# Optimization experiments

Hardware: AMD Instinct MI355X
Metric: run time of the kernel (lower is better)

Reference implementation:

```python
import jax, jax.numpy as jnp
import numpy as np

B, T, F, H = 256, 512, 64, 128


def _uniform(key, shape, stdv):
    return jax.random.uniform(key, shape, jnp.float32, -stdv, stdv)


def setup_inputs() -> dict:
    key = jax.random.key(0)
    ks = jax.random.split(key, 24)
    values = jax.random.normal(ks[0], (B, T, F), jnp.float32)
    masks = (jax.random.uniform(ks[1], (B, T, F)) < 0.8).astype(jnp.float32)
    deltas = jax.random.uniform(ks[2], (B, T, F), jnp.float32)
    labels = (jax.random.uniform(ks[3], (B, 1)) < 0.5).astype(jnp.float32)
    is_train = (jax.random.uniform(ks[4], (B, 1)) < 0.8).astype(jnp.float32)
    sH = 1.0 / np.sqrt(H)
    sF = 1.0 / np.sqrt(F)
    # temp_decay_h: Linear F -> H (stdv = 1/sqrt(out) per reset_parameters)
    W_dh = _uniform(ks[5], (H, F), sH); b_dh = _uniform(ks[6], (H,), sH)
    # temp_decay_x: diag F -> F
    W_dx = _uniform(ks[7], (F, F), sF); b_dx = _uniform(ks[8], (F,), sF)
    # hist_reg: Linear H -> F (torch Linear stdv = 1/sqrt(in))
    W_hr = _uniform(ks[9], (F, H), sH); b_hr = _uniform(ks[10], (F,), sH)
    # feat_reg: F -> F with zeroed diagonal mask
    W_fr = _uniform(ks[11], (F, F), sF); b_fr = _uniform(ks[12], (F,), sF)
    # weight_combine: Linear 2F -> F
    s2F = 1.0 / np.sqrt(2 * F)
    W_wc = _uniform(ks[13], (F, 2 * F), s2F); b_wc = _uniform(ks[14], (F,), s2F)
    # LSTMCell(2F, H): torch init uniform(-1/sqrt(H), 1/sqrt(H)), gate order i,f,g,o
    W_ih = _uniform(ks[15], (4 * H, 2 * F), sH); b_ih = _uniform(ks[16], (4 * H,), sH)
    W_hh = _uniform(ks[17], (4 * H, H), sH); b_hh = _uniform(ks[18], (4 * H,), sH)
    # out: Linear H -> 1
    W_out = _uniform(ks[19], (1, H), sH); b_out = _uniform(ks[20], (1,), sH)
    return dict(values=values, masks=masks, deltas=deltas, labels=labels, is_train=is_train,
                W_dh=W_dh, b_dh=b_dh, W_dx=W_dx, b_dx=b_dx, W_hr=W_hr, b_hr=b_hr,
                W_fr=W_fr, b_fr=b_fr, W_wc=W_wc, b_wc=b_wc,
                W_ih=W_ih, b_ih=b_ih, W_hh=W_hh, b_hh=b_hh, W_out=W_out, b_out=b_out)


def _forward(values, masks, deltas, labels, is_train,
             W_dh, b_dh, W_dx, b_dx, W_hr, b_hr, W_fr, b_fr, W_wc, b_wc,
             W_ih, b_ih, W_hh, b_hh, W_out, b_out):
    eps = 1e-5
    w_dx_diag = jnp.diagonal(W_dx)            # diag mask: W * I
    W_fr_m = W_fr * (1.0 - jnp.eye(F, dtype=W_fr.dtype))  # zero diagonal

    def step(carry, xs):
        h, c, x_loss = carry
        x, m, d = xs                           # each [B, F]
        gamma_h = jnp.exp(-jax.nn.relu(d @ W_dh.T + b_dh))   # [B, H]
        gamma_x = jnp.exp(-jax.nn.relu(d * w_dx_diag + b_dx))  # [B, F]
        h = h * gamma_h
        x_h = h @ W_hr.T + b_hr                # [B, F]
        msum = jnp.sum(m) + eps
        x_loss = x_loss + jnp.sum(jnp.abs(x - x_h) * m) / msum
        x_c = m * x + (1.0 - m) * x_h
        z_h = x_c @ W_fr_m.T + b_fr
        x_loss = x_loss + jnp.sum(jnp.abs(x - z_h) * m) / msum
        alpha = jnp.concatenate([gamma_x, m], axis=1) @ W_wc.T + b_wc
        c_h = alpha * z_h + (1.0 - alpha) * x_h
        x_loss = x_loss + jnp.sum(jnp.abs(x - c_h) * m) / msum
        c_c = m * x + (1.0 - m) * c_h
        inp = jnp.concatenate([c_c, m], axis=1)   # [B, 2F]
        gates = inp @ W_ih.T + b_ih + h @ W_hh.T + b_hh  # [B, 4H]
        i, f, g, o = jnp.split(gates, 4, axis=1)
        c = jax.nn.sigmoid(f) * c + jax.nn.sigmoid(i) * jnp.tanh(g)
        h = jax.nn.sigmoid(o) * jnp.tanh(c)
        return (h, c, x_loss), c_c

    h0 = jnp.zeros((values.shape[0], H), values.dtype)
    c0 = jnp.zeros((values.shape[0], H), values.dtype)
    xs = (jnp.swapaxes(values, 0, 1), jnp.swapaxes(masks, 0, 1), jnp.swapaxes(deltas, 0, 1))
    (h, c, x_loss), imps = jax.lax.scan(step, (h0, c0, jnp.float32(0.0)), xs)
    imputations = jnp.swapaxes(imps, 0, 1)     # [B, T, F]
    y_h = h @ W_out.T + b_out                  # [B, 1] logits
    # stable BCE with logits (matches torch reference formula)
    max_val = jnp.maximum(-y_h, 0.0)
    y_l = y_h - y_h * labels + max_val + jnp.log(jnp.exp(-max_val) + jnp.exp(-y_h - max_val))
    y_loss = jnp.sum(y_l * is_train) / (jnp.sum(is_train) + eps)
    loss = x_loss / T + y_loss * 0.3
    predictions = jax.nn.sigmoid(y_h)
    return loss, predictions, imputations


def reference(values, masks, deltas, labels, is_train,
              W_dh, b_dh, W_dx, b_dx, W_hr, b_hr, W_fr, b_fr, W_wc, b_wc,
              W_ih, b_ih, W_hh, b_hh, W_out, b_out):
    return _forward(values, masks, deltas, labels, is_train,
                    W_dh, b_dh, W_dx, b_dx, W_hr, b_hr, W_fr, b_fr, W_wc, b_wc,
                    W_ih, b_ih, W_hh, b_hh, W_out, b_out)
```

## Files before the change

### kernel.cpp

```cpp
#include <hip/hip_runtime.h>
#include <hip/hip_fp16.h>


#define NBATCH 256
#define NT 512
#define NF 64
#define NH 128

#define WHH_OFF   0u
#define WIH_OFF   131072u
#define WHR_OFF   262144u
#define WFR_OFF   278528u
#define INVMS_OFF 286720u
#define ISTR_OFF  288768u
#define GH_OFF    294912u
#define AL_OFF    33849344u

typedef _Float16 half2_t __attribute__((ext_vector_type(2)));

__device__ __forceinline__ unsigned pack2(float a, float b) {
    __half2 h = __floats2half2_rn(a, b);
    return __builtin_bit_cast(unsigned, h);
}

__device__ __forceinline__ float dot2f(unsigned w, unsigned a, float acc) {
#if __has_builtin(__builtin_amdgcn_fdot2)
    return __builtin_amdgcn_fdot2(__builtin_bit_cast(half2_t, w),
                                  __builtin_bit_cast(half2_t, a), acc, false);
#else
    float2 wf = __half22float2(__builtin_bit_cast(__half2, w));
    float2 af = __half22float2(__builtin_bit_cast(__half2, a));
    return acc + wf.x * af.x + wf.y * af.y;
#endif
}

__device__ __forceinline__ float sigm(float x) { return 1.f / (1.f + __expf(-x)); }
__device__ __forceinline__ float tanh_fast(float x) { return 1.f - 2.f / (__expf(2.f * x) + 1.f); }

__global__ __launch_bounds__(256) void prep_w(const float* __restrict__ Whh,
                                              const float* __restrict__ Wih,
                                              const float* __restrict__ Whr,
                                              const float* __restrict__ Wfr,
                                              unsigned* __restrict__ wsu) {
    int o = blockIdx.x * 256 + threadIdx.x;
    float v0, v1;
    if (o < 32768) {
        int c = o & 3, r = (o >> 2) & 511, cb = o >> 11;
        int col = 8 * cb + 2 * c;
        v0 = Whh[r * 128 + col]; v1 = Whh[r * 128 + col + 1];
    } else if (o < 65536) {
        int o2 = o - 32768;
        int c = o2 & 3, r = (o2 >> 2) & 511, cb = o2 >> 11;
        int col = 8 * cb + 2 * c;
        v0 = Wih[r * 128 + col]; v1 = Wih[r * 128 + col + 1];
    } else if (o < 69632) {
        int o3 = o - 65536;
        int c = o3 & 3, f = (o3 >> 2) & 63, cb = o3 >> 8;
        int col = 8 * cb + 2 * c;
        v0 = Whr[f * 128 + col]; v1 = Whr[f * 128 + col + 1];
    } else if (o < 71680) {
        int o4 = o - 69632;
        int c = o4 & 3, f = (o4 >> 2) & 63, cb = o4 >> 8;
        int col = 8 * cb + 2 * c;
        v0 = (col == f) ? 0.f : Wfr[f * 64 + col];
        v1 = (col + 1 == f) ? 0.f : Wfr[f * 64 + col + 1];
    } else {
        return;
    }
    wsu[o] = pack2(v0, v1);
}

__global__ __launch_bounds__(256) void prep_msum(const float* __restrict__ masks,
                                                 const float* __restrict__ is_train,
                                                 float* __restrict__ invms,
                                                 float* __restrict__ inv_istr,
                                                 float* __restrict__ d_out0) {
    __shared__ float red[256];
    int tid = threadIdx.x;
    int t = blockIdx.x;
    if (t < NT) {
        int f = tid & 63, br = tid >> 6;
        float s = 0.f;
        for (int i = 0; i < 64; i++) {
            int b = br + i * 4;
            s += masks[((size_t)b * NT + t) * NF + f];
        }
        red[tid] = s;
        __syncthreads();
        for (int off = 128; off > 0; off >>= 1) {
            if (tid < off) red[tid] += red[tid + off];
            __syncthreads();
        }
        if (tid == 0) invms[t] = 1.f / (red[0] + 1e-5f);
    } else {
        red[tid] = is_train[tid];
        __syncthreads();
        for (int off = 128; off > 0; off >>= 1) {
            if (tid < off) red[tid] += red[tid + off];
            __syncthreads();
        }
        if (tid == 0) {
            *inv_istr = 1.f / (red[0] + 1e-5f);
            *d_out0 = 0.f;
        }
    }
}

__global__ __launch_bounds__(256) void ga_kernel(const float* __restrict__ deltas,
                                                 const float* __restrict__ masks,
                                                 const float* __restrict__ Wdh,
                                                 const float* __restrict__ bdh,
                                                 const float* __restrict__ Wdx,
                                                 const float* __restrict__ bdx,
                                                 const float* __restrict__ Wwc,
                                                 const float* __restrict__ bwc,
                                                 __half* __restrict__ gh_all,
                                                 __half* __restrict__ al_all) {
    __shared__ unsigned wdhpk[32 * 128];
    __shared__ unsigned wwcpk[64 * 64];
    __shared__ float sbdh[128], sbdx[64], swdx[64], sbwc[64];
    __shared__ float dbuf[64];
    __shared__ __align__(16) unsigned dpk[32], gxpk[32], mpk2[32];
    int tid = threadIdx.x;

    for (int o = tid; o < 4096; o += 256) {
        int j = o & 127, k2 = o >> 7;
        wdhpk[o] = pack2(Wdh[j * 64 + 2 * k2], Wdh[j * 64 + 2 * k2 + 1]);
    }
    for (int o = tid; o < 4096; o += 256) {
        int f = o & 63, k2 = o >> 6;
        wwcpk[o] = pack2(Wwc[f * 128 + 2 * k2], Wwc[f * 128 + 2 * k2 + 1]);
    }
    if (tid < 128) sbdh[tid] = bdh[tid];
    if (tid < 64) {
        sbdx[tid] = bdx[tid];
        swdx[tid] = Wdx[tid * 65];
        sbwc[tid] = bwc[tid];
    }
    __syncthreads();

    for (int i = 0; i < 32; i++) {
        int p = blockIdx.x * 32 + i;
        if (tid < 32) {
            float2 dv = ((const float2*)(deltas + (size_t)p * NF))[tid];
            dbuf[2 * tid] = dv.x; dbuf[2 * tid + 1] = dv.y;
            dpk[tid] = pack2(dv.x, dv.y);
        } else if (tid < 64) {
            int q = tid - 32;
            float2 mv = ((const float2*)(masks + (size_t)p * NF))[q];
            mpk2[q] = pack2(mv.x, mv.y);
        }
        __syncthreads();
        if (tid < 64) {
            float gx = __expf(-fmaxf(dbuf[tid] * swdx[tid] + sbdx[tid], 0.f));
            float oth = __shfl_xor(gx, 1);
            if (!(tid & 1)) gxpk[tid >> 1] = pack2(gx, oth);
        }
        __syncthreads();
        if (tid < 128) {
            float a0 = sbdh[tid], a1 = 0.f;
            #pragma unroll
            for (int k8 = 0; k8 < 8; k8++) {
                uint4 dp = *(const uint4*)&dpk[4 * k8];
                a0 = dot2f(wdhpk[(4 * k8 + 0) * 128 + tid], dp.x, a0);
                a1 = dot2f(wdhpk[(4 * k8 + 1) * 128 + tid], dp.y, a1);
                a0 = dot2f(wdhpk[(4 * k8 + 2) * 128 + tid], dp.z, a0);
                a1 = dot2f(wdhpk[(4 * k8 + 3) * 128 + tid], dp.w, a1);
            }
            gh_all[(size_t)p * NH + tid] = __float2half(__expf(-fmaxf(a0 + a1, 0.f)));
        } else if (tid < 192) {
            int f = tid - 128;
            float a0 = sbwc[f], a1 = 0.f;
            #pragma unroll
            for (int k8 = 0; k8 < 8; k8++) {
                uint4 gp = *(const uint4*)&gxpk[4 * k8];
                a0 = dot2f(wwcpk[(4 * k8 + 0) * 64 + f], gp.x, a0);
                a1 = dot2f(wwcpk[(4 * k8 + 1) * 64 + f], gp.y, a1);
                a0 = dot2f(wwcpk[(4 * k8 + 2) * 64 + f], gp.z, a0);
                a1 = dot2f(wwcpk[(4 * k8 + 3) * 64 + f], gp.w, a1);
            }
            #pragma unroll
            for (int k8 = 0; k8 < 8; k8++) {
                uint4 mp = *(const uint4*)&mpk2[4 * k8];
                a0 = dot2f(wwcpk[(32 + 4 * k8 + 0) * 64 + f], mp.x, a0);
                a1 = dot2f(wwcpk[(32 + 4 * k8 + 1) * 64 + f], mp.y, a1);
                a0 = dot2f(wwcpk[(32 + 4 * k8 + 2) * 64 + f], mp.z, a0);
                a1 = dot2f(wwcpk[(32 + 4 * k8 + 3) * 64 + f], mp.w, a1);
            }
            al_all[(size_t)p * NF + f] = __float2half(a0 + a1);
        }
        __syncthreads();
    }
}

__global__ __launch_bounds__(512, 2) void main_kernel(
    const float* __restrict__ values, const float* __restrict__ masks,
    const float* __restrict__ labels, const float* __restrict__ is_train,
    const float* __restrict__ b_hr, const float* __restrict__ b_fr,
    const float* __restrict__ b_ih, const float* __restrict__ b_hh,
    const float* __restrict__ W_out, const float* __restrict__ b_out,
    const uint4* __restrict__ whh_ws, const uint4* __restrict__ wih_ws,
    const uint4* __restrict__ whr_ws, const uint4* __restrict__ wfr_ws,
    const float* __restrict__ invms, const float* __restrict__ inv_istr,
    const __half* __restrict__ gh_all, const __half* __restrict__ al_all,
    float* __restrict__ d_out) {
    __shared__ uint4 wfr4[8 * 64];
    __shared__ float sbhr[64], sbfr[64];
    __shared__ __align__(16) unsigned hpk[64];
    __shared__ float xp[512];
    __shared__ float mbuf[64], xbuf[64], albuf[64];
    __shared__ __align__(16) unsigned mpk[32], xcpk[32], ccpk[32];
    __shared__ __align__(16) unsigned ghpk[64];
    __shared__ float hfin[128];
    __shared__ float sinvt;

    const int tid = threadIdx.x;
    const int b = blockIdx.x;
    const int s = tid & 3;
    const int cq = tid >> 2;
    const int kg = tid >> 6;
    const int fl = tid & 63;

    uint4 whh_q[16];
    uint4 wihc_q[8];
    uint4 wihm_q[8];
    float bg4[4];
    #pragma unroll
    for (int g = 0; g < 4; g++) {
        int r = g * 128 + cq;
        #pragma unroll
        for (int j = 0; j < 4; j++) whh_q[g * 4 + j] = whh_ws[(4 * s + j) * 512 + r];
        #pragma unroll
        for (int j = 0; j < 2; j++) {
            wihc_q[g * 2 + j] = wih_ws[(2 * s + j) * 512 + r];
            wihm_q[g * 2 + j] = wih_ws[(8 + 2 * s + j) * 512 + r];
        }
        bg4[g] = b_ih[r] + b_hh[r];
    }
    uint4 whr_pa = whr_ws[(2 * kg) * 64 + fl];
    uint4 whr_pb = whr_ws[(2 * kg + 1) * 64 + fl];
    wfr4[tid] = wfr_ws[tid];
    if (tid < 64) { sbhr[tid] = b_hr[tid]; sbfr[tid] = b_fr[tid]; hpk[tid] = 0u; }

    const float* vp = values + (size_t)b * NT * NF;
    const float* mp = masks + (size_t)b * NT * NF;
    const __half* alp = al_all + (size_t)b * NT * NF;
    const unsigned* ghu = (const unsigned*)(gh_all + (size_t)b * NT * NH);
    float* imp = d_out + 257 + (size_t)b * NT * NF;

    float creg = 0.f;
    float lloss = 0.f;
    float hacc4[4] = {0.f, 0.f, 0.f, 0.f};
    float macc4[4] = {0.f, 0.f, 0.f, 0.f};

    float xn = 0.f, aln = 0.f, invtn = 0.f;
    float2 mn = make_float2(0.f, 0.f);
    unsigned ghA = 0u, ghB = 0u;
    if (tid >= 256 && tid < 320) {
        int q = tid - 256;
        xn = vp[q];
        aln = __half2float(alp[q]);
        if (q == 0) invtn = invms[0];
    } else if (tid >= 320 && tid < 352) {
        mn = ((const float2*)mp)[tid - 320];
    } else if (tid >= 352 && tid < 416) {
        int q = tid - 352;
        ghA = ghu[64 + q];
        ghB = ghu[128 + q];
    }
    __syncthreads();

    for (int t = 0; t < NT; t++) {
        if (tid >= 256 && tid < 320) {
            int q = tid - 256;
            xbuf[q] = xn; albuf[q] = aln;
            if (q == 0) sinvt = invtn;
        } else if (tid >= 320 && tid < 352) {
            int q = tid - 320;
            mbuf[2 * q] = mn.x; mbuf[2 * q + 1] = mn.y;
            mpk[q] = pack2(mn.x, mn.y);
        }
        {
            int tn = (t + 1 < NT) ? (t + 1) : (NT - 1);
            if (tid >= 256 && tid < 320) {
                int q = tid - 256;
                xn = vp[tn * NF + q];
                aln = __half2float(alp[tn * NF + q]);
                if (q == 0) invtn = invms[tn];
            } else if (tid >= 320 && tid < 352) {
                mn = ((const float2*)(mp + tn * NF))[tid - 320];
            }
        }
        #pragma unroll
        for (int g = 0; g < 4; g++) {
            float u0 = 0.f, u1 = 0.f;
            #pragma unroll
            for (int j = 0; j < 4; j++) {
                uint4 hq = *(const uint4*)&hpk[16 * s + 4 * j];
                uint4 w = whh_q[g * 4 + j];
                u0 = dot2f(w.x, hq.x, u0); u1 = dot2f(w.y, hq.y, u1);
                u0 = dot2f(w.z, hq.z, u0); u1 = dot2f(w.w, hq.w, u1);
            }
            hacc4[g] = u0 + u1;
        }
        {
            uint4 hpa = *(const uint4*)&hpk[8 * kg];
            uint4 hpb = *(const uint4*)&hpk[8 * kg + 4];
            float p0, p1;
            p0 = dot2f(whr_pa.x, hpa.x, 0.f); p1 = dot2f(whr_pa.y, hpa.y, 0.f);
            p0 = dot2f(whr_pa.z, hpa.z, p0);  p1 = dot2f(whr_pa.w, hpa.w, p1);
            p0 = dot2f(whr_pb.x, hpb.x, p0);  p1 = dot2f(whr_pb.y, hpb.y, p1);
            p0 = dot2f(whr_pb.z, hpb.z, p0);  p1 = dot2f(whr_pb.w, hpb.w, p1);
            xp[tid] = p0 + p1;
        }
        __syncthreads();

        if (tid < 64) {
            __builtin_amdgcn_s_setprio(1);
            float xh = sbhr[fl];
            #pragma unroll
            for (int g8 = 0; g8 < 8; g8++) xh += xp[g8 * 64 + fl];
            float xv = xbuf[fl], mv = mbuf[fl], av = albuf[fl], it = sinvt;
            float xc = mv * xv + (1.f - mv) * xh;
            float oth = __shfl_xor(xc, 1);
            if (!(fl & 1)) xcpk[fl >> 1] = pack2(xc, oth);
            float b0 = sbfr[fl], b1 = 0.f;
            #pragma unroll
            for (int k4 = 0; k4 < 8; k4++) {
                uint4 w = wfr4[k4 * 64 + fl];
                uint4 xq = *(const uint4*)&xcpk[4 * k4];
                b0 = dot2f(w.x, xq.x, b0); b1 = dot2f(w.y, xq.y, b1);
                b0 = dot2f(w.z, xq.z, b0); b1 = dot2f(w.w, xq.w, b1);
            }
            float zh = b0 + b1;
            float ch = av * zh + (1.f - av) * xh;
            float cc = mv * xv + (1.f - mv) * ch;
            imp[t * NF + fl] = cc;
            lloss += (fabsf(xv - xh) + fabsf(xv - zh) + fabsf(xv - ch)) * mv * it;
            oth = __shfl_xor(cc, 1);
            if (!(fl & 1)) ccpk[fl >> 1] = pack2(cc, oth);
            __builtin_amdgcn_s_setprio(0);
        } else {
            if (tid >= 352 && tid < 416) {
                int q = tid - 352;
                ghpk[q] = ghA;
                ghA = ghB;
                int tg = (t + 3 < NT) ? (t + 3) : (NT - 1);
                ghB = ghu[(size_t)tg * 64 + q];
            }
            uint4 mq0 = *(const uint4*)&mpk[8 * s];
            uint4 mq1 = *(const uint4*)&mpk[8 * s + 4];
            #pragma unroll
            for (int g = 0; g < 4; g++) {
                uint4 wa = wihm_q[g * 2], wb = wihm_q[g * 2 + 1];
                float u0 = dot2f(wa.x, mq0.x, 0.f), u1 = dot2f(wa.y, mq0.y, 0.f);
                u0 = dot2f(wa.z, mq0.z, u0); u1 = dot2f(wa.w, mq0.w, u1);
                u0 = dot2f(wb.x, mq1.x, u0); u1 = dot2f(wb.y, mq1.y, u1);
                u0 = dot2f(wb.z, mq1.z, u0); u1 = dot2f(wb.w, mq1.w, u1);
                macc4[g] = u0 + u1;
            }
        }
        __syncthreads();

        {
            if (tid < 64) {
                uint4 mq0 = *(const uint4*)&mpk[8 * s];
                uint4 mq1 = *(const uint4*)&mpk[8 * s + 4];
                #pragma unroll
                for (int g = 0; g < 4; g++) {
                    uint4 wa = wihm_q[g * 2], wb = wihm_q[g * 2 + 1];
                    float u0 = dot2f(wa.x, mq0.x, 0.f), u1 = dot2f(wa.y, mq0.y, 0.f);
                    u0 = dot2f(wa.z, mq0.z, u0); u1 = dot2f(wa.w, mq0.w, u1);
                    u0 = dot2f(wb.x, mq1.x, u0); u1 = dot2f(wb.y, mq1.y, u1);
                    u0 = dot2f(wb.z, mq1.z, u0); u1 = dot2f(wb.w, mq1.w, u1);
                    macc4[g] = u0 + u1;
                }
            }
            uint4 cq0 = *(const uint4*)&ccpk[8 * s];
            uint4 cq1 = *(const uint4*)&ccpk[8 * s + 4];
            float gate[4];
            #pragma unroll
            for (int g = 0; g < 4; g++) {
                uint4 wa = wihc_q[g * 2], wb = wihc_q[g * 2 + 1];
                float u0 = dot2f(wa.x, cq0.x, 0.f), u1 = dot2f(wa.y, cq0.y, 0.f);
                u0 = dot2f(wa.z, cq0.z, u0); u1 = dot2f(wa.w, cq0.w, u1);
                u0 = dot2f(wb.x, cq1.x, u0); u1 = dot2f(wb.y, cq1.y, u1);
                u0 = dot2f(wb.z, cq1.z, u0); u1 = dot2f(wb.w, cq1.w, u1);
                float v = hacc4[g] + macc4[g] + (u0 + u1);
                v += __shfl_xor(v, 1);
                v += __shfl_xor(v, 2);
                gate[g] = v + bg4[g];
            }
            float cn = sigm(gate[1]) * creg + sigm(gate[0]) * tanh_fast(gate[2]);
            creg = cn;
            float hn = sigm(gate[3]) * tanh_fast(cn);
            float gm = __half2float(((const __half*)ghpk)[cq]);
            float hd = hn * gm;
            float oth = __shfl_xor(hd, 4);
            if (!(tid & 7)) hpk[tid >> 3] = pack2(hd, oth);
            if (t == NT - 1 && !(tid & 3)) hfin[cq] = hn;
        }
        __syncthreads();
    }

    if (tid < 64) {
        float ll = lloss;
        float yp = hfin[tid] * W_out[tid] + hfin[64 + tid] * W_out[64 + tid];
        #pragma unroll
        for (int off = 32; off > 0; off >>= 1) {
            ll += __shfl_down(ll, off);
            yp += __shfl_down(yp, off);
        }
        if (tid == 0) {
            float yh = yp + b_out[0];
            d_out[1 + b] = 1.f / (1.f + expf(-yh));
            float lab = labels[b], istr = is_train[b];
            float maxv = fmaxf(-yh, 0.f);
            float yl = yh - yh * lab + maxv + logf(expf(-maxv) + expf(-yh - maxv));
            atomicAdd(d_out, ll * (1.f / (float)NT) + 0.3f * yl * istr * (*inv_istr));
        }
    }
}

extern "C" void kernel_launch(void* const* d_in, const int* in_sizes, int n_in,
                              void* d_out, int out_size, void* d_ws, size_t ws_size,
                              hipStream_t stream) {
    const float* values = (const float*)d_in[0];
    const float* masks = (const float*)d_in[1];
    const float* deltas = (const float*)d_in[2];
    const float* labels = (const float*)d_in[3];
    const float* is_train = (const float*)d_in[4];
    const float* W_dh = (const float*)d_in[5];
    const float* b_dh = (const float*)d_in[6];
    const float* W_dx = (const float*)d_in[7];
    const float* b_dx = (const float*)d_in[8];
    const float* W_hr = (const float*)d_in[9];
    const float* b_hr = (const float*)d_in[10];
    const float* W_fr = (const float*)d_in[11];
    const float* b_fr = (const float*)d_in[12];
    const float* W_wc = (const float*)d_in[13];
    const float* b_wc = (const float*)d_in[14];
    const float* W_ih = (const float*)d_in[15];
    const float* b_ih = (const float*)d_in[16];
    const float* W_hh = (const float*)d_in[17];
    const float* b_hh = (const float*)d_in[18];
    const float* W_out = (const float*)d_in[19];
    const float* b_out = (const float*)d_in[20];

    char* ws = (char*)d_ws;
    unsigned* wsu = (unsigned*)d_ws;
    const uint4* whh_ws = (const uint4*)(ws + WHH_OFF);
    const uint4* wih_ws = (const uint4*)(ws + WIH_OFF);
    const uint4* whr_ws = (const uint4*)(ws + WHR_OFF);
    const uint4* wfr_ws = (const uint4*)(ws + WFR_OFF);
    float* invms = (float*)(ws + INVMS_OFF);
    float* inv_istr = (float*)(ws + ISTR_OFF);
    __half* gh_all = (__half*)(ws + GH_OFF);
    __half* al_all = (__half*)(ws + AL_OFF);
    float* out_f = (float*)d_out;

    prep_w<<<280, 256, 0, stream>>>(W_hh, W_ih, W_hr, W_fr, wsu);
    prep_msum<<<513, 256, 0, stream>>>(masks, is_train, invms, inv_istr, out_f);
    ga_kernel<<<4096, 256, 0, stream>>>(deltas, masks, W_dh, b_dh, W_dx, b_dx,
                                        W_wc, b_wc, gh_all, al_all);
    main_kernel<<<NBATCH, 512, 0, stream>>>(values, masks, labels, is_train,
                                            b_hr, b_fr, b_ih, b_hh, W_out, b_out,
                                            whh_ws, wih_ws, whr_ws, wfr_ws,
                                            invms, inv_istr, gh_all, al_all, out_f);
}
```

Measured before the change: 1.372 ms.

## Unroll timestep loop by four with batched input staging and DPP reductions

After: 1.289 ms. 1.06x faster.

```diff
diff --git a/kernel.cpp b/kernel.cpp
--- a/kernel.cpp
+++ b/kernel.cpp
@@ -36,6 +36,19 @@
 
 __device__ __forceinline__ float sigm(float x) { return 1.f / (1.f + __expf(-x)); }
 __device__ __forceinline__ float tanh_fast(float x) { return 1.f - 2.f / (__expf(2.f * x) + 1.f); }
+
+__device__ __forceinline__ float quad_add_x1(float v) {
+    int r = __builtin_amdgcn_update_dpp(0, __builtin_bit_cast(int, v),
+                                        0xB1 , 0xF, 0xF, true);
+    return v + __builtin_bit_cast(float, r);
+}
+__device__ __forceinline__ float quad_add_x2(float v) {
+    int r = __builtin_amdgcn_update_dpp(0, __builtin_bit_cast(int, v),
+                                        0x4E , 0xF, 0xF, true);
+    return v + __builtin_bit_cast(float, r);
+}
+
+#define KEEP4(u) asm volatile("" : "+v"(u.x), "+v"(u.y), "+v"(u.z), "+v"(u.w))
 
 __global__ __launch_bounds__(256) void prep_w(const float* __restrict__ Whh,
                                               const float* __restrict__ Wih,
@@ -206,13 +219,14 @@
     float* __restrict__ d_out) {
     __shared__ uint4 wfr4[8 * 64];
     __shared__ float sbhr[64], sbfr[64];
-    __shared__ __align__(16) unsigned hpk[64];
+    __shared__ __align__(16) __half hph[128];
     __shared__ float xp[512];
-    __shared__ float mbuf[64], xbuf[64], albuf[64];
-    __shared__ __align__(16) unsigned mpk[32], xcpk[32], ccpk[32];
-    __shared__ __align__(16) unsigned ghpk[64];
+    __shared__ float xbuf4[4][64], albuf4[4][64], mbuf4[4][64];
+    __shared__ __align__(16) unsigned mpk4[4][32];
+    __shared__ __align__(16) __half xcph[64], ccph[64];
+    __shared__ __align__(16) unsigned ghpk4[4][64];
+    __shared__ float invt4[4];
     __shared__ float hfin[128];
-    __shared__ float sinvt;
 
     const int tid = threadIdx.x;
     const int b = blockIdx.x;
@@ -240,7 +254,8 @@
     uint4 whr_pa = whr_ws[(2 * kg) * 64 + fl];
     uint4 whr_pb = whr_ws[(2 * kg + 1) * 64 + fl];
     wfr4[tid] = wfr_ws[tid];
-    if (tid < 64) { sbhr[tid] = b_hr[tid]; sbfr[tid] = b_fr[tid]; hpk[tid] = 0u; }
+    if (tid < 64) { sbhr[tid] = b_hr[tid]; sbfr[tid] = b_fr[tid]; }
+    if (tid < 128) hph[tid] = __float2half(0.f);
 
     const float* vp = values + (size_t)b * NT * NF;
     const float* mp = masks + (size_t)b * NT * NF;
@@ -252,120 +267,152 @@
     float lloss = 0.f;
     float hacc4[4] = {0.f, 0.f, 0.f, 0.f};
     float macc4[4] = {0.f, 0.f, 0.f, 0.f};
-
-    float xn = 0.f, aln = 0.f, invtn = 0.f;
-    float2 mn = make_float2(0.f, 0.f);
-    unsigned ghA = 0u, ghB = 0u;
+    float ccb0 = 0.f, ccb1 = 0.f, ccb2 = 0.f, ccb3 = 0.f;
+
+    float xr4[4] = {0.f, 0.f, 0.f, 0.f};
+    __half ar4[4] = {};
+    float ir4[4] = {0.f, 0.f, 0.f, 0.f};
+    float2 mr4[4] = {};
+    unsigned gr4[4] = {0u, 0u, 0u, 0u};
+
     if (tid >= 256 && tid < 320) {
         int q = tid - 256;
-        xn = vp[q];
-        aln = __half2float(alp[q]);
-        if (q == 0) invtn = invms[0];
+        #pragma unroll
+        for (int u = 0; u < 4; u++) {
+            xr4[u] = vp[u * NF + q];
+            ar4[u] = alp[u * NF + q];
+        }
+        if (q == 0) {
+            #pragma unroll
+            for (int u = 0; u < 4; u++) ir4[u] = invms[u];
+        }
     } else if (tid >= 320 && tid < 352) {
-        mn = ((const float2*)mp)[tid - 320];
+        int q = tid - 320;
+        #pragma unroll
+        for (int u = 0; u < 4; u++) mr4[u] = ((const float2*)(mp + u * NF))[q];
     } else if (tid >= 352 && tid < 416) {
         int q = tid - 352;
-        ghA = ghu[64 + q];
-        ghB = ghu[128 + q];
+        #pragma unroll
+        for (int u = 0; u < 4; u++) gr4[u] = ghu[(size_t)(u + 1) * 64 + q];
     }
     __syncthreads();
 
-    for (int t = 0; t < NT; t++) {
-        if (tid >= 256 && tid < 320) {
-            int q = tid - 256;
-            xbuf[q] = xn; albuf[q] = aln;
-            if (q == 0) sinvt = invtn;
-        } else if (tid >= 320 && tid < 352) {
-            int q = tid - 320;
-            mbuf[2 * q] = mn.x; mbuf[2 * q + 1] = mn.y;
-            mpk[q] = pack2(mn.x, mn.y);
-        }
-        {
-            int tn = (t + 1 < NT) ? (t + 1) : (NT - 1);
-            if (tid >= 256 && tid < 320) {
-                int q = tid - 256;
-                xn = vp[tn * NF + q];
-                aln = __half2float(alp[tn * NF + q]);
-                if (q == 0) invtn = invms[tn];
-            } else if (tid >= 320 && tid < 352) {
-                mn = ((const float2*)(mp + tn * NF))[tid - 320];
-            }
-        }
-        #pragma unroll
-        for (int g = 0; g < 4; g++) {
-            float u0 = 0.f, u1 = 0.f;
-            #pragma unroll
-            for (int j = 0; j < 4; j++) {
-                uint4 hq = *(const uint4*)&hpk[16 * s + 4 * j];
-                uint4 w = whh_q[g * 4 + j];
-                u0 = dot2f(w.x, hq.x, u0); u1 = dot2f(w.y, hq.y, u1);
-                u0 = dot2f(w.z, hq.z, u0); u1 = dot2f(w.w, hq.w, u1);
-            }
-            hacc4[g] = u0 + u1;
-        }
-        {
-            uint4 hpa = *(const uint4*)&hpk[8 * kg];
-            uint4 hpb = *(const uint4*)&hpk[8 * kg + 4];
-            float p0, p1;
-            p0 = dot2f(whr_pa.x, hpa.x, 0.f); p1 = dot2f(whr_pa.y, hpa.y, 0.f);
-            p0 = dot2f(whr_pa.z, hpa.z, p0);  p1 = dot2f(whr_pa.w, hpa.w, p1);
-            p0 = dot2f(whr_pb.x, hpb.x, p0);  p1 = dot2f(whr_pb.y, hpb.y, p1);
-            p0 = dot2f(whr_pb.z, hpb.z, p0);  p1 = dot2f(whr_pb.w, hpb.w, p1);
-            xp[tid] = p0 + p1;
-        }
-        __syncthreads();
-
-        if (tid < 64) {
-            __builtin_amdgcn_s_setprio(1);
-            float xh = sbhr[fl];
-            #pragma unroll
-            for (int g8 = 0; g8 < 8; g8++) xh += xp[g8 * 64 + fl];
-            float xv = xbuf[fl], mv = mbuf[fl], av = albuf[fl], it = sinvt;
-            float xc = mv * xv + (1.f - mv) * xh;
-            float oth = __shfl_xor(xc, 1);
-            if (!(fl & 1)) xcpk[fl >> 1] = pack2(xc, oth);
-            float b0 = sbfr[fl], b1 = 0.f;
-            #pragma unroll
-            for (int k4 = 0; k4 < 8; k4++) {
-                uint4 w = wfr4[k4 * 64 + fl];
-                uint4 xq = *(const uint4*)&xcpk[4 * k4];
-                b0 = dot2f(w.x, xq.x, b0); b1 = dot2f(w.y, xq.y, b1);
-                b0 = dot2f(w.z, xq.z, b0); b1 = dot2f(w.w, xq.w, b1);
-            }
-            float zh = b0 + b1;
-            float ch = av * zh + (1.f - av) * xh;
-            float cc = mv * xv + (1.f - mv) * ch;
-            imp[t * NF + fl] = cc;
-            lloss += (fabsf(xv - xh) + fabsf(xv - zh) + fabsf(xv - ch)) * mv * it;
-            oth = __shfl_xor(cc, 1);
-            if (!(fl & 1)) ccpk[fl >> 1] = pack2(cc, oth);
-            __builtin_amdgcn_s_setprio(0);
-        } else {
-            if (tid >= 352 && tid < 416) {
-                int q = tid - 352;
-                ghpk[q] = ghA;
-                ghA = ghB;
-                int tg = (t + 3 < NT) ? (t + 3) : (NT - 1);
-                ghB = ghu[(size_t)tg * 64 + q];
-            }
-            uint4 mq0 = *(const uint4*)&mpk[8 * s];
-            uint4 mq1 = *(const uint4*)&mpk[8 * s + 4];
+    for (int tb = 0; tb < NT; tb += 4) {
+        #pragma unroll
+        for (int i = 0; i < 16; i++) { KEEP4(whh_q[i]); }
+        #pragma unroll
+        for (int i = 0; i < 8; i++) { KEEP4(wihc_q[i]); KEEP4(wihm_q[i]); }
+        KEEP4(whr_pa); KEEP4(whr_pb);
+
+        #pragma unroll
+        for (int j = 0; j < 4; j++) {
+            const int t = tb + j;
+            if (j == 0) {
+                if (tid >= 256 && tid < 320) {
+                    int q = tid - 256;
+                    #pragma unroll
+                    for (int u = 0; u < 4; u++) {
+                        xbuf4[u][q] = xr4[u];
+                        albuf4[u][q] = __half2float(ar4[u]);
+                    }
+                    if (q == 0) {
+                        #pragma unroll
+                        for (int u = 0; u < 4; u++) invt4[u] = ir4[u];
+                    }
+                    #pragma unroll
+                    for (int u = 0; u < 4; u++) {
+                        int tn = tb + 4 + u; if (tn > NT - 1) tn = NT - 1;
+                        xr4[u] = vp[tn * NF + q];
+                        ar4[u] = alp[tn * NF + q];
+                    }
+                    if (q == 0) {
+                        #pragma unroll
+                        for (int u = 0; u < 4; u++) {
+                            int tn = tb + 4 + u; if (tn > NT - 1) tn = NT - 1;
+                            ir4[u] = invms[tn];
+                        }
+                    }
+                } else if (tid >= 320 && tid < 352) {
+                    int q = tid - 320;
+                    #pragma unroll
+                    for (int u = 0; u < 4; u++) {
+                        mbuf4[u][2 * q] = mr4[u].x; mbuf4[u][2 * q + 1] = mr4[u].y;
+                        mpk4[u][q] = pack2(mr4[u].x, mr4[u].y);
+                    }
+                    #pragma unroll
+                    for (int u = 0; u < 4; u++) {
+                        int tn = tb + 4 + u; if (tn > NT - 1) tn = NT - 1;
+                        mr4[u] = ((const float2*)(mp + tn * NF))[q];
+                    }
+                } else if (tid >= 352 && tid < 416) {
+                    int q = tid - 352;
+                    #pragma unroll
+                    for (int u = 0; u < 4; u++) ghpk4[u][q] = gr4[u];
+                    #pragma unroll
+                    for (int u = 0; u < 4; u++) {
+                        int tg = tb + 5 + u; if (tg > NT - 1) tg = NT - 1;
+                        gr4[u] = ghu[(size_t)tg * 64 + q];
+                    }
+                }
+            }
             #pragma unroll
             for (int g = 0; g < 4; g++) {
-                uint4 wa = wihm_q[g * 2], wb = wihm_q[g * 2 + 1];
-                float u0 = dot2f(wa.x, mq0.x, 0.f), u1 = dot2f(wa.y, mq0.y, 0.f);
-                u0 = dot2f(wa.z, mq0.z, u0); u1 = dot2f(wa.w, mq0.w, u1);
-                u0 = dot2f(wb.x, mq1.x, u0); u1 = dot2f(wb.y, mq1.y, u1);
-                u0 = dot2f(wb.z, mq1.z, u0); u1 = dot2f(wb.w, mq1.w, u1);
-                macc4[g] = u0 + u1;
-            }
-        }
-        __syncthreads();
-
-        {
+                float u0 = 0.f, u1 = 0.f;
+                #pragma unroll
+                for (int jj = 0; jj < 4; jj++) {
+                    uint4 hq = *(const uint4*)&hph[32 * s + 8 * jj];
+                    uint4 w = whh_q[g * 4 + jj];
+                    u0 = dot2f(w.x, hq.x, u0); u1 = dot2f(w.y, hq.y, u1);
+                    u0 = dot2f(w.z, hq.z, u0); u1 = dot2f(w.w, hq.w, u1);
+                }
+                hacc4[g] = u0 + u1;
+            }
+            {
+                uint4 hpa = *(const uint4*)&hph[16 * kg];
+                uint4 hpb = *(const uint4*)&hph[16 * kg + 8];
+                float p0, p1;
+                p0 = dot2f(whr_pa.x, hpa.x, 0.f); p1 = dot2f(whr_pa.y, hpa.y, 0.f);
+                p0 = dot2f(whr_pa.z, hpa.z, p0);  p1 = dot2f(whr_pa.w, hpa.w, p1);
+                p0 = dot2f(whr_pb.x, hpb.x, p0);  p1 = dot2f(whr_pb.y, hpb.y, p1);
+                p0 = dot2f(whr_pb.z, hpb.z, p0);  p1 = dot2f(whr_pb.w, hpb.w, p1);
+                xp[tid] = p0 + p1;
+            }
+            __syncthreads();
+
             if (tid < 64) {
-                uint4 mq0 = *(const uint4*)&mpk[8 * s];
-                uint4 mq1 = *(const uint4*)&mpk[8 * s + 4];
+                __builtin_amdgcn_s_setprio(1);
+                float xh = sbhr[fl];
+                #pragma unroll
+                for (int g8 = 0; g8 < 8; g8++) xh += xp[g8 * 64 + fl];
+                float xv = xbuf4[j][fl], mv = mbuf4[j][fl];
+                float av = albuf4[j][fl], it = invt4[j];
+                float xc = mv * xv + (1.f - mv) * xh;
+                xcph[fl] = __float2half(xc);
+                float b0 = sbfr[fl], b1 = 0.f;
+                #pragma unroll
+                for (int k4 = 0; k4 < 8; k4++) {
+                    uint4 w = wfr4[k4 * 64 + fl];
+                    uint4 xq = *(const uint4*)&xcph[8 * k4];
+                    b0 = dot2f(w.x, xq.x, b0); b1 = dot2f(w.y, xq.y, b1);
+                    b0 = dot2f(w.z, xq.z, b0); b1 = dot2f(w.w, xq.w, b1);
+                }
+                float zh = b0 + b1;
+                float ch = av * zh + (1.f - av) * xh;
+                float cc = mv * xv + (1.f - mv) * ch;
+                if (j == 0) ccb0 = cc; else if (j == 1) ccb1 = cc;
+                else if (j == 2) ccb2 = cc; else ccb3 = cc;
+                lloss += (fabsf(xv - xh) + fabsf(xv - zh) + fabsf(xv - ch)) * mv * it;
+                ccph[fl] = __float2half(cc);
+                if (j == 3) {
+                    imp[(tb + 0) * NF + fl] = ccb0;
+                    imp[(tb + 1) * NF + fl] = ccb1;
+                    imp[(tb + 2) * NF + fl] = ccb2;
+                    imp[(tb + 3) * NF + fl] = ccb3;
+                }
+                __builtin_amdgcn_s_setprio(0);
+            } else {
+                uint4 mq0 = *(const uint4*)&mpk4[j][8 * s];
+                uint4 mq1 = *(const uint4*)&mpk4[j][8 * s + 4];
                 #pragma unroll
                 for (int g = 0; g < 4; g++) {
                     uint4 wa = wihm_q[g * 2], wb = wihm_q[g * 2 + 1];
@@ -376,31 +423,47 @@
                     macc4[g] = u0 + u1;
                 }
             }
-            uint4 cq0 = *(const uint4*)&ccpk[8 * s];
-            uint4 cq1 = *(const uint4*)&ccpk[8 * s + 4];
-            float gate[4];
-            #pragma unroll
-            for (int g = 0; g < 4; g++) {
-                uint4 wa = wihc_q[g * 2], wb = wihc_q[g * 2 + 1];
-                float u0 = dot2f(wa.x, cq0.x, 0.f), u1 = dot2f(wa.y, cq0.y, 0.f);
-                u0 = dot2f(wa.z, cq0.z, u0); u1 = dot2f(wa.w, cq0.w, u1);
-                u0 = dot2f(wb.x, cq1.x, u0); u1 = dot2f(wb.y, cq1.y, u1);
-                u0 = dot2f(wb.z, cq1.z, u0); u1 = dot2f(wb.w, cq1.w, u1);
-                float v = hacc4[g] + macc4[g] + (u0 + u1);
-                v += __shfl_xor(v, 1);
-                v += __shfl_xor(v, 2);
-                gate[g] = v + bg4[g];
-            }
-            float cn = sigm(gate[1]) * creg + sigm(gate[0]) * tanh_fast(gate[2]);
-            creg = cn;
-            float hn = sigm(gate[3]) * tanh_fast(cn);
-            float gm = __half2float(((const __half*)ghpk)[cq]);
-            float hd = hn * gm;
-            float oth = __shfl_xor(hd, 4);
-            if (!(tid & 7)) hpk[tid >> 3] = pack2(hd, oth);
-            if (t == NT - 1 && !(tid & 3)) hfin[cq] = hn;
-        }
-        __syncthreads();
+            __syncthreads();
+
+            {
+                if (tid < 64) {
+                    uint4 mq0 = *(const uint4*)&mpk4[j][8 * s];
+                    uint4 mq1 = *(const uint4*)&mpk4[j][8 * s + 4];
+                    #pragma unroll
+                    for (int g = 0; g < 4; g++) {
+                        uint4 wa = wihm_q[g * 2], wb = wihm_q[g * 2 + 1];
+                        float u0 = dot2f(wa.x, mq0.x, 0.f), u1 = dot2f(wa.y, mq0.y, 0.f);
+                        u0 = dot2f(wa.z, mq0.z, u0); u1 = dot2f(wa.w, mq0.w, u1);
+                        u0 = dot2f(wb.x, mq1.x, u0); u1 = dot2f(wb.y, mq1.y, u1);
+                        u0 = dot2f(wb.z, mq1.z, u0); u1 = dot2f(wb.w, mq1.w, u1);
+                        macc4[g] = u0 + u1;
+                    }
+                }
+                uint4 cq0 = *(const uint4*)&ccph[16 * s];
+                uint4 cq1 = *(const uint4*)&ccph[16 * s + 8];
+                float gate[4];
+                #pragma unroll
+                for (int g = 0; g < 4; g++) {
+                    uint4 wa = wihc_q[g * 2], wb = wihc_q[g * 2 + 1];
+                    float u0 = dot2f(wa.x, cq0.x, 0.f), u1 = dot2f(wa.y, cq0.y, 0.f);
+                    u0 = dot2f(wa.z, cq0.z, u0); u1 = dot2f(wa.w, cq0.w, u1);
+                    u0 = dot2f(wb.x, cq1.x, u0); u1 = dot2f(wb.y, cq1.y, u1);
+                    u0 = dot2f(wb.z, cq1.z, u0); u1 = dot2f(wb.w, cq1.w, u1);
+                    float v = hacc4[g] + macc4[g] + (u0 + u1);
+                    v = quad_add_x1(v);
+                    v = quad_add_x2(v);
+                    gate[g] = v + bg4[g];
+                }
+                float cn = sigm(gate[1]) * creg + sigm(gate[0]) * tanh_fast(gate[2]);
+                creg = cn;
+                float hn = sigm(gate[3]) * tanh_fast(cn);
+                float gm = __half2float(((const __half*)&ghpk4[j][0])[cq]);
+                float hd = hn * gm;
+                if (s == 0) hph[cq] = __float2half(hd);
+                if (t == NT - 1 && s == 0) hfin[cq] = hn;
+            }
+            __syncthreads();
+        }
     }
 
     if (tid < 64) {
```
